# Performance work log

Hardware: AMD Instinct MI355X
Metric: run time of the kernel (lower is better)

## Reference

```python
import jax, jax.numpy as jnp
import numpy as np

N_NODES = 100000
N_EDGES = 1600000
F_IN, H1, H2, N_CLS = 512, 180, 120, 40
NEG_SLOPE = 0.01  # F.leaky_relu default


def setup_inputs() -> dict:
    key = jax.random.key(0)
    ks = jax.random.split(key, 8)
    x = jax.random.normal(ks[0], (N_NODES, F_IN), dtype=jnp.float32)
    edge_index = jax.random.randint(ks[1], (2, N_EDGES), 0, N_NODES, dtype=jnp.int64)
    W1 = jax.random.normal(ks[2], (F_IN, H1), dtype=jnp.float32) / np.sqrt(F_IN)
    b1 = jnp.zeros((H1,), dtype=jnp.float32)
    W2 = jax.random.normal(ks[3], (H1, H2), dtype=jnp.float32) / np.sqrt(H1)
    b2 = jnp.zeros((H2,), dtype=jnp.float32)
    W3 = jax.random.normal(ks[4], (H2, N_CLS), dtype=jnp.float32) / np.sqrt(H2)
    b3 = jnp.zeros((N_CLS,), dtype=jnp.float32)
    return {"x": x, "edge_index": edge_index, "W1": W1, "b1": b1,
            "W2": W2, "b2": b2, "W3": W3, "b3": b3}


def _add_self_loops(edge_index, n):
    loop = jnp.arange(n, dtype=edge_index.dtype)
    src = jnp.concatenate([edge_index[0], loop])
    dst = jnp.concatenate([edge_index[1], loop])
    return src, dst


def _gcn_conv(h, src, dst, norm, W, b, n):
    # PyG GCNConv: linear transform first, then normalized scatter-add at dst.
    h = h @ W  # [N, out]
    msg = norm[:, None] * h[src]  # gather at source, per-edge scale
    out = jax.ops.segment_sum(msg, dst, num_segments=n)  # scatter-add at dest
    return out + b


def reference(x, edge_index, W1, b1, W2, b2, W3, b3):
    n = x.shape[0]
    src, dst = _add_self_loops(edge_index, n)
    # symmetric normalization deg^-1/2 * deg^-1/2 on self-loop-augmented graph
    ones = jnp.ones(dst.shape[0], dtype=x.dtype)
    deg = jax.ops.segment_sum(ones, dst, num_segments=n)
    dinv = jnp.where(deg > 0, jax.lax.rsqrt(deg), 0.0)
    norm = dinv[src] * dinv[dst]  # [E+N]

    h = _gcn_conv(x, src, dst, norm, W1, b1, n)
    h = jnp.where(h >= 0, h, NEG_SLOPE * h)
    h = _gcn_conv(h, src, dst, norm, W2, b2, n)
    h = jnp.where(h >= 0, h, NEG_SLOPE * h)
    logits = h @ W3 + b3
    return jax.nn.log_softmax(logits, axis=1)
```

## Files before the change

kernel.cpp:

```cpp
#include <hip/hip_runtime.h>
#include <math.h>

typedef __attribute__((ext_vector_type(8))) short short8;
typedef __attribute__((ext_vector_type(4))) float f32x4;

static constexpr int F_IN = 512;
static constexpr int H1V = 180, H1P = 192;
static constexpr int H2V = 120, H2P = 128;
static constexpr int NC  = 40,  NCP = 64;

__device__ inline unsigned f2bf(float f) {
    unsigned u = __float_as_uint(f);
    return (u + 0x7fffu + ((u >> 16) & 1u)) >> 16;
}
__device__ inline unsigned cvtpk(float lo, float hi) {
    unsigned r;
    asm("v_cvt_pk_bf16_f32 %0, %1, %2" : "=v"(r) : "v"(lo), "v"(hi));
    return r;
}
#define BLO(u) __uint_as_float((u) << 16)
#define BHI(u) __uint_as_float((u) & 0xffff0000u)

__device__ inline void gload_lds16(const void* gsrc, void* ldst) {
    __builtin_amdgcn_global_load_lds(
        (const __attribute__((address_space(1))) void*)gsrc,
        (__attribute__((address_space(3))) void*)ldst, 16, 0, 0);
}

__global__ void k_detect(const int* __restrict__ ei, int* __restrict__ flag) {
    int i = blockIdx.x * 256 + threadIdx.x;
    if (ei[2 * i + 1] != 0) flag[0] = 0;
}

__global__ void k_hist(const int* __restrict__ ei, int E, const int* __restrict__ flag,
                       int* __restrict__ deg, int* __restrict__ rank) {
    int e = blockIdx.x * 256 + threadIdx.x;
    if (e >= E) return;
    int d = flag[0] ? ei[2 * E + 2 * e] : ei[E + e];
    rank[e] = atomicAdd(&deg[d], 1);
}

__global__ void k_dinv(const int* __restrict__ deg, float* __restrict__ dinv, int n) {
    int i = blockIdx.x * 256 + threadIdx.x;
    if (i < n) dinv[i] = rsqrtf((float)(deg[i] + 1));
}

__global__ void k_scan1(const int* __restrict__ deg, int* __restrict__ rp,
                        int* __restrict__ bsum, int n) {
    __shared__ int s[256];
    int t = threadIdx.x;
    int base = blockIdx.x * 1024 + t * 4;
    int v0 = (base + 0 < n) ? deg[base + 0] : 0;
    int v1 = (base + 1 < n) ? deg[base + 1] : 0;
    int v2 = (base + 2 < n) ? deg[base + 2] : 0;
    int v3 = (base + 3 < n) ? deg[base + 3] : 0;
    int sum = v0 + v1 + v2 + v3;
    s[t] = sum;
    __syncthreads();
    for (int off = 1; off < 256; off <<= 1) {
        int x = (t >= off) ? s[t - off] : 0;
        __syncthreads();
        s[t] += x;
        __syncthreads();
    }
    int run = s[t] - sum;
    if (t == 255) bsum[blockIdx.x] = s[255];
    if (base + 0 < n) rp[base + 0] = run; run += v0;
    if (base + 1 < n) rp[base + 1] = run; run += v1;
    if (base + 2 < n) rp[base + 2] = run; run += v2;
    if (base + 3 < n) rp[base + 3] = run;
}

__global__ void k_scan2(int* __restrict__ bsum, int nb) {
    __shared__ int s[128];
    int t = threadIdx.x;
    int v = (t < nb) ? bsum[t] : 0;
    s[t] = v;
    __syncthreads();
    for (int off = 1; off < 128; off <<= 1) {
        int x = (t >= off) ? s[t - off] : 0;
        __syncthreads();
        s[t] += x;
        __syncthreads();
    }
    if (t < nb) bsum[t] = s[t] - v;
}

__global__ void k_scan3(const int* __restrict__ bsum, int* __restrict__ rp,
                        int n, int E) {
    int i = blockIdx.x * 256 + threadIdx.x;
    if (i < n) {
        rp[i] = rp[i] + bsum[i >> 10];
    } else if (i == n) {
        rp[n] = E;
    }
}

__global__ __launch_bounds__(256) void k_fill(const int* __restrict__ ei, int E,
                                              const int* __restrict__ flag,
                                              const int* __restrict__ rp,
                                              const int* __restrict__ rank,
                                              int* __restrict__ csr,
                                              int bw, int chunk) {
    int bkt = blockIdx.x & 7;
    int lo = bkt * bw, hi = lo + bw;
    int ch = blockIdx.x >> 3;
    int e0 = ch * chunk;
    int e1 = min(E, e0 + chunk);
    bool i64 = flag[0] != 0;
    for (int e = e0 + (int)threadIdx.x; e < e1; e += 256) {
        int d = i64 ? ei[2 * E + 2 * e] : ei[E + e];
        if (d >= lo && d < hi) {
            int s = i64 ? ei[2 * e] : ei[e];
            csr[rp[d] + rank[e]] = s;
        }
    }
}

__global__ void k_pad(const float* __restrict__ src, float* __restrict__ dst,
                      int KS, int NS, int ND, int total) {
    int i = blockIdx.x * 256 + threadIdx.x;
    if (i >= total) return;
    int k = i / ND, nn = i % ND;
    dst[i] = (k < KS && nn < NS) ? src[k * NS + nn] : 0.0f;
}

__global__ void k_padneg(const float* __restrict__ src, float* __restrict__ dst,
                         int NS, int ND) {
    int i = threadIdx.x;
    if (i < ND) dst[i] = (i < NS) ? src[i] : -1e30f;
}

__global__ void k_prepw(const float* __restrict__ src, unsigned short* __restrict__ dst,
                        int KS, int NS, int KD, int ND) {
    int i = blockIdx.x * 256 + threadIdx.x;
    if (i >= KD * ND) return;
    int k = i / ND, c = i % ND;
    float v = (k < KS && c < NS) ? src[k * NS + c] : 0.0f;
    dst[(size_t)(k >> 3) * ND * 8 + c * 8 + (k & 7)] = (unsigned short)f2bf(v);
}

__global__ __launch_bounds__(512) void k_gemm1(const float* __restrict__ X,
                                               const short8* __restrict__ Bs,
                                               const float* __restrict__ dinv,
                                               unsigned short* __restrict__ Hout,
                                               int M) {
    __shared__ float ldsf[8192];
    char* lds = (char*)ldsf;
    int t = threadIdx.x;
    int w = t >> 6, l = t & 63;
    int lr = l & 15, kg = l >> 4;
    int wr = w >> 2, wc = w & 3;
    int row0 = blockIdx.x * 128;
    int colb = wc * 48;

    f32x4 acc[4][3];
#pragma unroll
    for (int m = 0; m < 4; ++m)
#pragma unroll
        for (int nn = 0; nn < 3; ++nn) acc[m][nn] = (f32x4){0.f, 0.f, 0.f, 0.f};

    auto stage = [&](int kb, int buf) {
#pragma unroll
        for (int j = 0; j < 2; ++j) {
            int o = j * 8192 + t * 16;
            int row = o >> 7;
            int col4 = ((o >> 4) & 7) ^ (row & 7);
            int rowg = row0 + row;
            if (rowg >= M) rowg = M - 1;
            gload_lds16(X + (size_t)rowg * F_IN + kb + col4 * 4,
                        lds + buf * 16384 + j * 8192 + w * 1024);
        }
    };

    stage(0, 0);
    __syncthreads();

    for (int ts = 0; ts < 16; ++ts) {
        int cur = ts & 1;
        if (ts < 15) stage((ts + 1) * 32, cur ^ 1);
        short8 b[3];
#pragma unroll
        for (int nn = 0; nn < 3; ++nn)
            b[nn] = Bs[(size_t)(ts * 4 + kg) * H1P + colb + nn * 16 + lr];
        short8 a[4];
#pragma unroll
        for (int m = 0; m < 4; ++m) {
            int row = wr * 64 + m * 16 + lr;
            char* base = lds + cur * 16384 + row * 128;
            float4 v0 = *(const float4*)(base + (((2 * kg + 0) ^ (row & 7)) * 16));
            float4 v1 = *(const float4*)(base + (((2 * kg + 1) ^ (row & 7)) * 16));
            union { unsigned u[4]; short8 s; } cu;
            cu.u[0] = cvtpk(v0.x, v0.y);
            cu.u[1] = cvtpk(v0.z, v0.w);
            cu.u[2] = cvtpk(v1.x, v1.y);
            cu.u[3] = cvtpk(v1.z, v1.w);
            a[m] = cu.s;
        }
#pragma unroll
        for (int m = 0; m < 4; ++m)
#pragma unroll
            for (int nn = 0; nn < 3; ++nn)
                acc[m][nn] = __builtin_amdgcn_mfma_f32_16x16x32_bf16(a[m], b[nn], acc[m][nn], 0, 0, 0);
        __syncthreads();
    }

#pragma unroll
    for (int m = 0; m < 4; ++m) {
        int r4 = row0 + wr * 64 + m * 16 + kg * 4;
#pragma unroll
        for (int j = 0; j < 4; ++j) {
            int grow = r4 + j;
            if (grow < M) {
                float dv = dinv[grow];
#pragma unroll
                for (int nn = 0; nn < 3; ++nn)
                    Hout[(size_t)grow * H1P + colb + nn * 16 + lr] =
                        (unsigned short)f2bf(acc[m][nn][j] * dv);
            }
        }
    }
}

__global__ __launch_bounds__(512) void k_gemm2(const unsigned short* __restrict__ A,
                                               const short8* __restrict__ Bs,
                                               const float* __restrict__ dinv,
                                               unsigned short* __restrict__ Hout,
                                               int M) {
    __shared__ unsigned short ldsu[16384];
    char* lds = (char*)ldsu;
    int t = threadIdx.x;
    int w = t >> 6, l = t & 63;
    int lr = l & 15, kg = l >> 4;
    int wr = w >> 2, wc = w & 3;
    int row0 = blockIdx.x * 128;
    int colb = wc * 32;

    f32x4 acc[4][2];
#pragma unroll
    for (int m = 0; m < 4; ++m)
#pragma unroll
        for (int nn = 0; nn < 2; ++nn) acc[m][nn] = (f32x4){0.f, 0.f, 0.f, 0.f};

    auto stage = [&](int kb, int buf) {
#pragma unroll
        for (int j = 0; j < 2; ++j) {
            int o = j * 8192 + t * 16;
            int row = o >> 7;
            int chunk = ((o >> 4) & 7) ^ (row & 7);
            int rowg = row0 + row;
            if (rowg >= M) rowg = M - 1;
            gload_lds16(A + (size_t)rowg * H1P + kb + chunk * 8,
                        lds + buf * 16384 + j * 8192 + w * 1024);
        }
    };

    stage(0, 0);
    __syncthreads();

    for (int ts = 0; ts < 3; ++ts) {
        int cur = ts & 1;
        if (ts < 2) stage((ts + 1) * 64, cur ^ 1);
        short8 b[2][2];
#pragma unroll
        for (int kk = 0; kk < 2; ++kk)
#pragma unroll
            for (int nn = 0; nn < 2; ++nn)
                b[kk][nn] = Bs[(size_t)(ts * 8 + kk * 4 + kg) * H2P + colb + nn * 16 + lr];
        short8 a[2][4];
#pragma unroll
        for (int kk = 0; kk < 2; ++kk)
#pragma unroll
            for (int m = 0; m < 4; ++m) {
                int row = wr * 64 + m * 16 + lr;
                a[kk][m] = *(const short8*)(lds + cur * 16384 + row * 128 +
                                            (((kk * 4 + kg) ^ (row & 7)) * 16));
            }
#pragma unroll
        for (int kk = 0; kk < 2; ++kk)
#pragma unroll
            for (int m = 0; m < 4; ++m)
#pragma unroll
                for (int nn = 0; nn < 2; ++nn)
                    acc[m][nn] = __builtin_amdgcn_mfma_f32_16x16x32_bf16(a[kk][m], b[kk][nn], acc[m][nn], 0, 0, 0);
        __syncthreads();
    }

#pragma unroll
    for (int m = 0; m < 4; ++m) {
        int r4 = row0 + wr * 64 + m * 16 + kg * 4;
#pragma unroll
        for (int j = 0; j < 4; ++j) {
            int grow = r4 + j;
            if (grow < M) {
                float dv = dinv[grow];
#pragma unroll
                for (int nn = 0; nn < 2; ++nn)
                    Hout[(size_t)grow * H2P + colb + nn * 16 + lr] =
                        (unsigned short)f2bf(acc[m][nn][j] * dv);
            }
        }
    }
}

template <int CH, int OUTBF>
__global__ __launch_bounds__(256) void k_gat(const uint2* __restrict__ H,
                                             const float* __restrict__ dinv,
                                             const int* __restrict__ rp,
                                             const int* __restrict__ csr,
                                             const float* __restrict__ bias,
                                             void* __restrict__ outv, int n) {
    int wv = threadIdx.x >> 6, l = threadIdx.x & 63;
    int i = blockIdx.x * 4 + wv;
    if (i >= n) return;
    bool act = l < CH;
    int c = act ? l : 0;
    const uint2* Hr = H + c;

    float a0, a1, a2, a3;
    {
        uint2 v = Hr[(size_t)i * CH];
        a0 = BLO(v.x); a1 = BHI(v.x); a2 = BLO(v.y); a3 = BHI(v.y);
    }
    float p0 = 0.f, p1 = 0.f, p2 = 0.f, p3 = 0.f;

    int e0 = rp[i], e1 = rp[i + 1];
    int e = e0;
    for (; e + 3 < e1; e += 4) {
        int s0 = csr[e], s1 = csr[e + 1], s2 = csr[e + 2], s3 = csr[e + 3];
        uint2 va = Hr[(size_t)s0 * CH];
        uint2 vb = Hr[(size_t)s1 * CH];
        uint2 vc = Hr[(size_t)s2 * CH];
        uint2 vd = Hr[(size_t)s3 * CH];
        a0 += BLO(va.x); a1 += BHI(va.x); a2 += BLO(va.y); a3 += BHI(va.y);
        p0 += BLO(vb.x); p1 += BHI(vb.x); p2 += BLO(vb.y); p3 += BHI(vb.y);
        a0 += BLO(vc.x); a1 += BHI(vc.x); a2 += BLO(vc.y); a3 += BHI(vc.y);
        p0 += BLO(vd.x); p1 += BHI(vd.x); p2 += BLO(vd.y); p3 += BHI(vd.y);
    }
    for (; e < e1; ++e) {
        int s0 = csr[e];
        uint2 va = Hr[(size_t)s0 * CH];
        a0 += BLO(va.x); a1 += BHI(va.x); a2 += BLO(va.y); a3 += BHI(va.y);
    }
    a0 += p0; a1 += p1; a2 += p2; a3 += p3;

    float di = dinv[i];
    float4 bb = *(const float4*)(bias + 4 * c);
    float o0 = fmaf(di, a0, bb.x);
    float o1 = fmaf(di, a1, bb.y);
    float o2 = fmaf(di, a2, bb.z);
    float o3 = fmaf(di, a3, bb.w);
    o0 = o0 >= 0.f ? o0 : 0.01f * o0;
    o1 = o1 >= 0.f ? o1 : 0.01f * o1;
    o2 = o2 >= 0.f ? o2 : 0.01f * o2;
    o3 = o3 >= 0.f ? o3 : 0.01f * o3;
    if (act) {
        if (OUTBF) {
            uint2 r;
            r.x = (f2bf(o1) << 16) | f2bf(o0);
            r.y = (f2bf(o3) << 16) | f2bf(o2);
            ((uint2*)outv)[(size_t)i * CH + c] = r;
        } else {
            ((float4*)outv)[(size_t)i * CH + c] = make_float4(o0, o1, o2, o3);
        }
    }
}

__global__ __launch_bounds__(256) void k_gat2(const uint2* __restrict__ H,
                                              const float* __restrict__ dinv,
                                              const int* __restrict__ rp,
                                              const int* __restrict__ csr,
                                              const float* __restrict__ bias,
                                              uint2* __restrict__ out, int n) {
    int wv = threadIdx.x >> 6, l = threadIdx.x & 63;
    int half = l >> 5, c = l & 31;
    int i = blockIdx.x * 8 + wv * 2 + half;
    if (i >= n) return;
    const uint2* Hr = H + c;

    float a0, a1, a2, a3;
    {
        uint2 v = Hr[(size_t)i * 32];
        a0 = BLO(v.x); a1 = BHI(v.x); a2 = BLO(v.y); a3 = BHI(v.y);
    }
    float p0 = 0.f, p1 = 0.f, p2 = 0.f, p3 = 0.f;

    int e0 = rp[i], e1 = rp[i + 1];
    int e = e0;
    for (; e + 3 < e1; e += 4) {
        int s0 = csr[e], s1 = csr[e + 1], s2 = csr[e + 2], s3 = csr[e + 3];
        uint2 va = Hr[(size_t)s0 * 32];
        uint2 vb = Hr[(size_t)s1 * 32];
        uint2 vc = Hr[(size_t)s2 * 32];
        uint2 vd = Hr[(size_t)s3 * 32];
        a0 += BLO(va.x); a1 += BHI(va.x); a2 += BLO(va.y); a3 += BHI(va.y);
        p0 += BLO(vb.x); p1 += BHI(vb.x); p2 += BLO(vb.y); p3 += BHI(vb.y);
        a0 += BLO(vc.x); a1 += BHI(vc.x); a2 += BLO(vc.y); a3 += BHI(vc.y);
        p0 += BLO(vd.x); p1 += BHI(vd.x); p2 += BLO(vd.y); p3 += BHI(vd.y);
    }
    for (; e < e1; ++e) {
        int s0 = csr[e];
        uint2 va = Hr[(size_t)s0 * 32];
        a0 += BLO(va.x); a1 += BHI(va.x); a2 += BLO(va.y); a3 += BHI(va.y);
    }
    a0 += p0; a1 += p1; a2 += p2; a3 += p3;

    float di = dinv[i];
    float4 bb = *(const float4*)(bias + 4 * c);
    float o0 = fmaf(di, a0, bb.x);
    float o1 = fmaf(di, a1, bb.y);
    float o2 = fmaf(di, a2, bb.z);
    float o3 = fmaf(di, a3, bb.w);
    o0 = o0 >= 0.f ? o0 : 0.01f * o0;
    o1 = o1 >= 0.f ? o1 : 0.01f * o1;
    o2 = o2 >= 0.f ? o2 : 0.01f * o2;
    o3 = o3 >= 0.f ? o3 : 0.01f * o3;
    uint2 r;
    r.x = (f2bf(o1) << 16) | f2bf(o0);
    r.y = (f2bf(o3) << 16) | f2bf(o2);
    out[(size_t)i * 32 + c] = r;
}

__global__ __launch_bounds__(256) void k_out(const unsigned short* __restrict__ H,
                                             const short8* __restrict__ Bs,
                                             const float* __restrict__ b3p,
                                             float* __restrict__ out, int M) {
    int t = threadIdx.x;
    int w = t >> 6, l = t & 63;
    int lr = l & 15, kg = l >> 4;
    int row0 = blockIdx.x * 64 + w * 16;

    f32x4 acc[4];
#pragma unroll
    for (int f = 0; f < 4; ++f) acc[f] = (f32x4){0.f, 0.f, 0.f, 0.f};

    int rowa = row0 + lr;
    if (rowa >= M) rowa = M - 1;
    const unsigned short* arow = H + (size_t)rowa * H2P;

#pragma unroll
    for (int ks = 0; ks < 4; ++ks) {
        short8 a = *(const short8*)(arow + ks * 32 + kg * 8);
#pragma unroll
        for (int f = 0; f < 4; ++f) {
            short8 b = Bs[(size_t)(ks * 4 + kg) * NCP + f * 16 + lr];
            acc[f] = __builtin_amdgcn_mfma_f32_16x16x32_bf16(a, b, acc[f], 0, 0, 0);
        }
    }

    float bl[4];
#pragma unroll
    for (int f = 0; f < 4; ++f) bl[f] = b3p[f * 16 + lr];

#pragma unroll
    for (int j = 0; j < 4; ++j) {
        int grow = row0 + kg * 4 + j;
        float lg[4];
#pragma unroll
        for (int f = 0; f < 4; ++f) lg[f] = acc[f][j] + bl[f];
        float m = fmaxf(fmaxf(lg[0], lg[1]), fmaxf(lg[2], lg[3]));
#pragma unroll
        for (int d = 1; d < 16; d <<= 1) m = fmaxf(m, __shfl_xor(m, d));
        float s = expf(lg[0] - m) + expf(lg[1] - m) + expf(lg[2] - m) + expf(lg[3] - m);
#pragma unroll
        for (int d = 1; d < 16; d <<= 1) s += __shfl_xor(s, d);
        float lse = m + logf(s);
        if (grow < M) {
#pragma unroll
            for (int f = 0; f < 4; ++f) {
                int c = f * 16 + lr;
                if (c < NC) out[(size_t)grow * NC + c] = lg[f] - lse;
            }
        }
    }
}

extern "C" void kernel_launch(void* const* d_in, const int* in_sizes, int n_in,
                              void* d_out, int out_size, void* d_ws, size_t ws_size,
                              hipStream_t stream) {
    const float* x  = (const float*)d_in[0];
    const int*   ei = (const int*)d_in[1];
    const float* W1 = (const float*)d_in[2];
    const float* b1 = (const float*)d_in[3];
    const float* W2 = (const float*)d_in[4];
    const float* b2 = (const float*)d_in[5];
    const float* W3 = (const float*)d_in[6];
    const float* b3 = (const float*)d_in[7];
    float* outp = (float*)d_out;

    int n = in_sizes[0] / F_IN;
    int E = in_sizes[1] / 2;

    char* p = (char*)d_ws;
    auto alloc = [&](size_t bytes) -> char* {
        char* r = p;
        p += (bytes + 511) & ~(size_t)511;
        return r;
    };
    int*            flag   = (int*)alloc(4);
    int*            deg    = (int*)alloc((size_t)n * 4);
    float*          dinv   = (float*)alloc((size_t)n * 4);
    int*            rp     = (int*)alloc((size_t)(n + 1) * 4);
    int*            bsum   = (int*)alloc(4096);
    int*            rank   = (int*)alloc((size_t)E * 4);
    int*            csr    = (int*)alloc((size_t)E * 4);
    unsigned short* W1s    = (unsigned short*)alloc((size_t)F_IN * H1P * 2);
    unsigned short* W2s    = (unsigned short*)alloc((size_t)H1P * H2P * 2);
    unsigned short* W3s    = (unsigned short*)alloc((size_t)H2P * NCP * 2);
    float*          b1p    = (float*)alloc(H1P * 4);
    float*          b2p    = (float*)alloc(H2P * 4);
    float*          b3p    = (float*)alloc(NCP * 4);
    unsigned short* h1     = (unsigned short*)alloc((size_t)n * H1P * 2);
    unsigned short* h1agg  = (unsigned short*)alloc((size_t)n * H1P * 2);
    unsigned short* h2     = (unsigned short*)alloc((size_t)n * H2P * 2);
    unsigned short* h2agg  = (unsigned short*)alloc((size_t)n * H2P * 2);

    hipMemsetAsync(flag, 1, 4, stream);
    hipMemsetAsync(deg, 0, (size_t)n * 4, stream);

    k_detect<<<16, 256, 0, stream>>>(ei, flag);

    int eb = (E + 255) / 256;
    k_hist<<<eb, 256, 0, stream>>>(ei, E, flag, deg, rank);
    k_dinv<<<(n + 255) / 256, 256, 0, stream>>>(deg, dinv, n);

    int nb = (n + 1023) / 1024;
    k_scan1<<<nb, 256, 0, stream>>>(deg, rp, bsum, n);
    k_scan2<<<1, 128, 0, stream>>>(bsum, nb);
    k_scan3<<<(n + 1 + 255) / 256, 256, 0, stream>>>(bsum, rp, n, E);

    int bw = (n + 7) / 8;
    int nch = 256;
    int chunk = (E + nch - 1) / nch;
    k_fill<<<nch * 8, 256, 0, stream>>>(ei, E, flag, rp, rank, csr, bw, chunk);

    k_prepw<<<(F_IN * H1P + 255) / 256, 256, 0, stream>>>(W1, W1s, F_IN, H1V, F_IN, H1P);
    k_prepw<<<(H1P * H2P + 255) / 256, 256, 0, stream>>>(W2, W2s, H1V, H2V, H1P, H2P);
    k_prepw<<<(H2P * NCP + 255) / 256, 256, 0, stream>>>(W3, W3s, H2V, NC, H2P, NCP);
    k_pad<<<1, 256, 0, stream>>>(b1, b1p, 1, H1V, H1P, H1P);
    k_pad<<<1, 256, 0, stream>>>(b2, b2p, 1, H2V, H2P, H2P);
    k_padneg<<<1, 64, 0, stream>>>(b3, b3p, NC, NCP);

    int gb = (n + 127) / 128;
    k_gemm1<<<gb, 512, 0, stream>>>(x, (const short8*)W1s, dinv, h1, n);
    k_gat<H1P / 4, 1><<<(n + 3) / 4, 256, 0, stream>>>((const uint2*)h1, dinv, rp, csr, b1p, h1agg, n);
    k_gemm2<<<gb, 512, 0, stream>>>(h1agg, (const short8*)W2s, dinv, h2, n);
    k_gat2<<<(n + 7) / 8, 256, 0, stream>>>((const uint2*)h2, dinv, rp, csr, b2p, (uint2*)h2agg, n);
    k_out<<<(n + 63) / 64, 256, 0, stream>>>(h2agg, (const short8*)W3s, b3p, outp, n);
}
```

Baseline: 395.2 us.

## Fuse neighbor aggregation with following GEMM via LDS staging

```diff
diff --git a/kernel.cpp b/kernel.cpp
--- a/kernel.cpp
+++ b/kernel.cpp
@@ -222,225 +222,169 @@
     }
 }
 
-__global__ __launch_bounds__(512) void k_gemm2(const unsigned short* __restrict__ A,
+__global__ __launch_bounds__(256) void k_fuse2(const uint2* __restrict__ H,
+                                               const float* __restrict__ dinv,
+                                               const int* __restrict__ rp,
+                                               const int* __restrict__ csr,
+                                               const float* __restrict__ bias,
                                                const short8* __restrict__ Bs,
-                                               const float* __restrict__ dinv,
                                                unsigned short* __restrict__ Hout,
-                                               int M) {
-    __shared__ unsigned short ldsu[16384];
-    char* lds = (char*)ldsu;
+                                               int n) {
+    __shared__ float ldsf[6400];
+    char* lds = (char*)ldsf;
     int t = threadIdx.x;
     int w = t >> 6, l = t & 63;
-    int lr = l & 15, kg = l >> 4;
-    int wr = w >> 2, wc = w & 3;
-    int row0 = blockIdx.x * 128;
-    int colb = wc * 32;
-
-    f32x4 acc[4][2];
-#pragma unroll
-    for (int m = 0; m < 4; ++m)
-#pragma unroll
-        for (int nn = 0; nn < 2; ++nn) acc[m][nn] = (f32x4){0.f, 0.f, 0.f, 0.f};
-
-    auto stage = [&](int kb, int buf) {
-#pragma unroll
-        for (int j = 0; j < 2; ++j) {
-            int o = j * 8192 + t * 16;
-            int row = o >> 7;
-            int chunk = ((o >> 4) & 7) ^ (row & 7);
-            int rowg = row0 + row;
-            if (rowg >= M) rowg = M - 1;
-            gload_lds16(A + (size_t)rowg * H1P + kb + chunk * 8,
-                        lds + buf * 16384 + j * 8192 + w * 1024);
-        }
-    };
-
-    stage(0, 0);
-    __syncthreads();
-
-    for (int ts = 0; ts < 3; ++ts) {
-        int cur = ts & 1;
-        if (ts < 2) stage((ts + 1) * 64, cur ^ 1);
-        short8 b[2][2];
-#pragma unroll
-        for (int kk = 0; kk < 2; ++kk)
-#pragma unroll
-            for (int nn = 0; nn < 2; ++nn)
-                b[kk][nn] = Bs[(size_t)(ts * 8 + kk * 4 + kg) * H2P + colb + nn * 16 + lr];
-        short8 a[2][4];
-#pragma unroll
-        for (int kk = 0; kk < 2; ++kk)
-#pragma unroll
-            for (int m = 0; m < 4; ++m) {
-                int row = wr * 64 + m * 16 + lr;
-                a[kk][m] = *(const short8*)(lds + cur * 16384 + row * 128 +
-                                            (((kk * 4 + kg) ^ (row & 7)) * 16));
-            }
-#pragma unroll
-        for (int kk = 0; kk < 2; ++kk)
-#pragma unroll
-            for (int m = 0; m < 4; ++m)
-#pragma unroll
-                for (int nn = 0; nn < 2; ++nn)
-                    acc[m][nn] = __builtin_amdgcn_mfma_f32_16x16x32_bf16(a[kk][m], b[kk][nn], acc[m][nn], 0, 0, 0);
-        __syncthreads();
-    }
-
-#pragma unroll
-    for (int m = 0; m < 4; ++m) {
-        int r4 = row0 + wr * 64 + m * 16 + kg * 4;
-#pragma unroll
-        for (int j = 0; j < 4; ++j) {
-            int grow = r4 + j;
-            if (grow < M) {
-                float dv = dinv[grow];
-#pragma unroll
-                for (int nn = 0; nn < 2; ++nn)
-                    Hout[(size_t)grow * H2P + colb + nn * 16 + lr] =
-                        (unsigned short)f2bf(acc[m][nn][j] * dv);
-            }
-        }
-    }
-}
-
-template <int CH, int OUTBF>
-__global__ __launch_bounds__(256) void k_gat(const uint2* __restrict__ H,
-                                             const float* __restrict__ dinv,
-                                             const int* __restrict__ rp,
-                                             const int* __restrict__ csr,
-                                             const float* __restrict__ bias,
-                                             void* __restrict__ outv, int n) {
-    int wv = threadIdx.x >> 6, l = threadIdx.x & 63;
-    int i = blockIdx.x * 4 + wv;
-    if (i >= n) return;
-    bool act = l < CH;
+    int row0 = blockIdx.x * 64;
+
+    bool act = l < 48;
     int c = act ? l : 0;
     const uint2* Hr = H + c;
-
-    float a0, a1, a2, a3;
-    {
-        uint2 v = Hr[(size_t)i * CH];
-        a0 = BLO(v.x); a1 = BHI(v.x); a2 = BLO(v.y); a3 = BHI(v.y);
-    }
-    float p0 = 0.f, p1 = 0.f, p2 = 0.f, p3 = 0.f;
-
-    int e0 = rp[i], e1 = rp[i + 1];
-    int e = e0;
-    for (; e + 3 < e1; e += 4) {
-        int s0 = csr[e], s1 = csr[e + 1], s2 = csr[e + 2], s3 = csr[e + 3];
-        uint2 va = Hr[(size_t)s0 * CH];
-        uint2 vb = Hr[(size_t)s1 * CH];
-        uint2 vc = Hr[(size_t)s2 * CH];
-        uint2 vd = Hr[(size_t)s3 * CH];
-        a0 += BLO(va.x); a1 += BHI(va.x); a2 += BLO(va.y); a3 += BHI(va.y);
-        p0 += BLO(vb.x); p1 += BHI(vb.x); p2 += BLO(vb.y); p3 += BHI(vb.y);
-        a0 += BLO(vc.x); a1 += BHI(vc.x); a2 += BLO(vc.y); a3 += BHI(vc.y);
-        p0 += BLO(vd.x); p1 += BHI(vd.x); p2 += BLO(vd.y); p3 += BHI(vd.y);
-    }
-    for (; e < e1; ++e) {
-        int s0 = csr[e];
-        uint2 va = Hr[(size_t)s0 * CH];
-        a0 += BLO(va.x); a1 += BHI(va.x); a2 += BLO(va.y); a3 += BHI(va.y);
-    }
-    a0 += p0; a1 += p1; a2 += p2; a3 += p3;
-
-    float di = dinv[i];
     float4 bb = *(const float4*)(bias + 4 * c);
-    float o0 = fmaf(di, a0, bb.x);
-    float o1 = fmaf(di, a1, bb.y);
-    float o2 = fmaf(di, a2, bb.z);
-    float o3 = fmaf(di, a3, bb.w);
-    o0 = o0 >= 0.f ? o0 : 0.01f * o0;
-    o1 = o1 >= 0.f ? o1 : 0.01f * o1;
-    o2 = o2 >= 0.f ? o2 : 0.01f * o2;
-    o3 = o3 >= 0.f ? o3 : 0.01f * o3;
-    if (act) {
-        if (OUTBF) {
+
+    for (int j = 0; j < 16; ++j) {
+        int i = row0 + w * 16 + j;
+        if (i >= n) break;
+        float a0, a1, a2, a3;
+        {
+            uint2 v = Hr[(size_t)i * 48];
+            a0 = BLO(v.x); a1 = BHI(v.x); a2 = BLO(v.y); a3 = BHI(v.y);
+        }
+        float p0 = 0.f, p1 = 0.f, p2 = 0.f, p3 = 0.f;
+        int e0 = rp[i], e1 = rp[i + 1];
+        int e = e0;
+        for (; e + 3 < e1; e += 4) {
+            int s0 = csr[e], s1 = csr[e + 1], s2 = csr[e + 2], s3 = csr[e + 3];
+            uint2 va = Hr[(size_t)s0 * 48];
+            uint2 vb = Hr[(size_t)s1 * 48];
+            uint2 vc = Hr[(size_t)s2 * 48];
+            uint2 vd = Hr[(size_t)s3 * 48];
+            a0 += BLO(va.x); a1 += BHI(va.x); a2 += BLO(va.y); a3 += BHI(va.y);
+            p0 += BLO(vb.x); p1 += BHI(vb.x); p2 += BLO(vb.y); p3 += BHI(vb.y);
+            a0 += BLO(vc.x); a1 += BHI(vc.x); a2 += BLO(vc.y); a3 += BHI(vc.y);
+            p0 += BLO(vd.x); p1 += BHI(vd.x); p2 += BLO(vd.y); p3 += BHI(vd.y);
+        }
+        for (; e < e1; ++e) {
+            int s0 = csr[e];
+            uint2 va = Hr[(size_t)s0 * 48];
+            a0 += BLO(va.x); a1 += BHI(va.x); a2 += BLO(va.y); a3 += BHI(va.y);
+        }
+        a0 += p0; a1 += p1; a2 += p2; a3 += p3;
+        float di = dinv[i];
+        float o0 = fmaf(di, a0, bb.x);
+        float o1 = fmaf(di, a1, bb.y);
+        float o2 = fmaf(di, a2, bb.z);
+        float o3 = fmaf(di, a3, bb.w);
+        o0 = o0 >= 0.f ? o0 : 0.01f * o0;
+        o1 = o1 >= 0.f ? o1 : 0.01f * o1;
+        o2 = o2 >= 0.f ? o2 : 0.01f * o2;
+        o3 = o3 >= 0.f ? o3 : 0.01f * o3;
+        if (act) {
             uint2 r;
             r.x = (f2bf(o1) << 16) | f2bf(o0);
             r.y = (f2bf(o3) << 16) | f2bf(o2);
-            ((uint2*)outv)[(size_t)i * CH + c] = r;
-        } else {
-            ((float4*)outv)[(size_t)i * CH + c] = make_float4(o0, o1, o2, o3);
-        }
-    }
-}
-
-__global__ __launch_bounds__(256) void k_gat2(const uint2* __restrict__ H,
-                                              const float* __restrict__ dinv,
-                                              const int* __restrict__ rp,
-                                              const int* __restrict__ csr,
-                                              const float* __restrict__ bias,
-                                              uint2* __restrict__ out, int n) {
-    int wv = threadIdx.x >> 6, l = threadIdx.x & 63;
-    int half = l >> 5, c = l & 31;
-    int i = blockIdx.x * 8 + wv * 2 + half;
-    if (i >= n) return;
-    const uint2* Hr = H + c;
-
-    float a0, a1, a2, a3;
-    {
-        uint2 v = Hr[(size_t)i * 32];
-        a0 = BLO(v.x); a1 = BHI(v.x); a2 = BLO(v.y); a3 = BHI(v.y);
-    }
-    float p0 = 0.f, p1 = 0.f, p2 = 0.f, p3 = 0.f;
-
-    int e0 = rp[i], e1 = rp[i + 1];
-    int e = e0;
-    for (; e + 3 < e1; e += 4) {
-        int s0 = csr[e], s1 = csr[e + 1], s2 = csr[e + 2], s3 = csr[e + 3];
-        uint2 va = Hr[(size_t)s0 * 32];
-        uint2 vb = Hr[(size_t)s1 * 32];
-        uint2 vc = Hr[(size_t)s2 * 32];
-        uint2 vd = Hr[(size_t)s3 * 32];
-        a0 += BLO(va.x); a1 += BHI(va.x); a2 += BLO(va.y); a3 += BHI(va.y);
-        p0 += BLO(vb.x); p1 += BHI(vb.x); p2 += BLO(vb.y); p3 += BHI(vb.y);
-        a0 += BLO(vc.x); a1 += BHI(vc.x); a2 += BLO(vc.y); a3 += BHI(vc.y);
-        p0 += BLO(vd.x); p1 += BHI(vd.x); p2 += BLO(vd.y); p3 += BHI(vd.y);
-    }
-    for (; e < e1; ++e) {
-        int s0 = csr[e];
-        uint2 va = Hr[(size_t)s0 * 32];
-        a0 += BLO(va.x); a1 += BHI(va.x); a2 += BLO(va.y); a3 += BHI(va.y);
-    }
-    a0 += p0; a1 += p1; a2 += p2; a3 += p3;
-
-    float di = dinv[i];
-    float4 bb = *(const float4*)(bias + 4 * c);
-    float o0 = fmaf(di, a0, bb.x);
-    float o1 = fmaf(di, a1, bb.y);
-    float o2 = fmaf(di, a2, bb.z);
-    float o3 = fmaf(di, a3, bb.w);
-    o0 = o0 >= 0.f ? o0 : 0.01f * o0;
-    o1 = o1 >= 0.f ? o1 : 0.01f * o1;
-    o2 = o2 >= 0.f ? o2 : 0.01f * o2;
-    o3 = o3 >= 0.f ? o3 : 0.01f * o3;
-    uint2 r;
-    r.x = (f2bf(o1) << 16) | f2bf(o0);
-    r.y = (f2bf(o3) << 16) | f2bf(o2);
-    out[(size_t)i * 32 + c] = r;
-}
-
-__global__ __launch_bounds__(256) void k_out(const unsigned short* __restrict__ H,
-                                             const short8* __restrict__ Bs,
-                                             const float* __restrict__ b3p,
-                                             float* __restrict__ out, int M) {
+            *(uint2*)(lds + (w * 16 + j) * 400 + c * 8) = r;
+        }
+    }
+    __syncthreads();
+
+    int lr = l & 15, kg = l >> 4;
+    f32x4 acc[8];
+#pragma unroll
+    for (int f = 0; f < 8; ++f) acc[f] = (f32x4){0.f, 0.f, 0.f, 0.f};
+
+#pragma unroll
+    for (int ks = 0; ks < 6; ++ks) {
+        short8 a = *(const short8*)(lds + (w * 16 + lr) * 400 + ks * 64 + kg * 16);
+#pragma unroll
+        for (int f = 0; f < 8; ++f) {
+            short8 b = Bs[(size_t)(ks * 4 + kg) * H2P + f * 16 + lr];
+            acc[f] = __builtin_amdgcn_mfma_f32_16x16x32_bf16(a, b, acc[f], 0, 0, 0);
+        }
+    }
+
+#pragma unroll
+    for (int j = 0; j < 4; ++j) {
+        int grow = row0 + w * 16 + kg * 4 + j;
+        if (grow < n) {
+            float dv = dinv[grow];
+#pragma unroll
+            for (int f = 0; f < 8; ++f)
+                Hout[(size_t)grow * H2P + f * 16 + lr] =
+                    (unsigned short)f2bf(acc[f][j] * dv);
+        }
+    }
+}
+
+__global__ __launch_bounds__(256) void k_fuse3(const uint2* __restrict__ H,
+                                               const float* __restrict__ dinv,
+                                               const int* __restrict__ rp,
+                                               const int* __restrict__ csr,
+                                               const float* __restrict__ bias,
+                                               const short8* __restrict__ Bs,
+                                               const float* __restrict__ b3p,
+                                               float* __restrict__ out, int n) {
+    __shared__ float ldsf[4352];
+    char* lds = (char*)ldsf;
     int t = threadIdx.x;
     int w = t >> 6, l = t & 63;
+    int row0 = blockIdx.x * 64;
+
+    int half = l >> 5, cc = l & 31;
+    const uint2* Hr = H + cc;
+    float4 bb = *(const float4*)(bias + 4 * cc);
+
+    for (int jj = 0; jj < 8; ++jj) {
+        int i = row0 + w * 16 + jj * 2 + half;
+        if (i >= n) continue;
+        float a0, a1, a2, a3;
+        {
+            uint2 v = Hr[(size_t)i * 32];
+            a0 = BLO(v.x); a1 = BHI(v.x); a2 = BLO(v.y); a3 = BHI(v.y);
+        }
+        float p0 = 0.f, p1 = 0.f, p2 = 0.f, p3 = 0.f;
+        int e0 = rp[i], e1 = rp[i + 1];
+        int e = e0;
+        for (; e + 3 < e1; e += 4) {
+            int s0 = csr[e], s1 = csr[e + 1], s2 = csr[e + 2], s3 = csr[e + 3];
+            uint2 va = Hr[(size_t)s0 * 32];
+            uint2 vb = Hr[(size_t)s1 * 32];
+            uint2 vc = Hr[(size_t)s2 * 32];
+            uint2 vd = Hr[(size_t)s3 * 32];
+            a0 += BLO(va.x); a1 += BHI(va.x); a2 += BLO(va.y); a3 += BHI(va.y);
+            p0 += BLO(vb.x); p1 += BHI(vb.x); p2 += BLO(vb.y); p3 += BHI(vb.y);
+            a0 += BLO(vc.x); a1 += BHI(vc.x); a2 += BLO(vc.y); a3 += BHI(vc.y);
+            p0 += BLO(vd.x); p1 += BHI(vd.x); p2 += BLO(vd.y); p3 += BHI(vd.y);
+        }
+        for (; e < e1; ++e) {
+            int s0 = csr[e];
+            uint2 va = Hr[(size_t)s0 * 32];
+            a0 += BLO(va.x); a1 += BHI(va.x); a2 += BLO(va.y); a3 += BHI(va.y);
+        }
+        a0 += p0; a1 += p1; a2 += p2; a3 += p3;
+        float di = dinv[i];
+        float o0 = fmaf(di, a0, bb.x);
+        float o1 = fmaf(di, a1, bb.y);
+        float o2 = fmaf(di, a2, bb.z);
+        float o3 = fmaf(di, a3, bb.w);
+        o0 = o0 >= 0.f ? o0 : 0.01f * o0;
+        o1 = o1 >= 0.f ? o1 : 0.01f * o1;
+        o2 = o2 >= 0.f ? o2 : 0.01f * o2;
+        o3 = o3 >= 0.f ? o3 : 0.01f * o3;
+        uint2 r;
+        r.x = (f2bf(o1) << 16) | f2bf(o0);
+        r.y = (f2bf(o3) << 16) | f2bf(o2);
+        *(uint2*)(lds + (w * 16 + jj * 2 + half) * 272 + cc * 8) = r;
+    }
+    __syncthreads();
+
     int lr = l & 15, kg = l >> 4;
-    int row0 = blockIdx.x * 64 + w * 16;
-
     f32x4 acc[4];
 #pragma unroll
     for (int f = 0; f < 4; ++f) acc[f] = (f32x4){0.f, 0.f, 0.f, 0.f};
 
-    int rowa = row0 + lr;
-    if (rowa >= M) rowa = M - 1;
-    const unsigned short* arow = H + (size_t)rowa * H2P;
-
 #pragma unroll
     for (int ks = 0; ks < 4; ++ks) {
-        short8 a = *(const short8*)(arow + ks * 32 + kg * 8);
+        short8 a = *(const short8*)(lds + (w * 16 + lr) * 272 + ks * 64 + kg * 16);
 #pragma unroll
         for (int f = 0; f < 4; ++f) {
             short8 b = Bs[(size_t)(ks * 4 + kg) * NCP + f * 16 + lr];
@@ -454,7 +398,7 @@
 
 #pragma unroll
     for (int j = 0; j < 4; ++j) {
-        int grow = row0 + kg * 4 + j;
+        int grow = row0 + w * 16 + kg * 4 + j;
         float lg[4];
 #pragma unroll
         for (int f = 0; f < 4; ++f) lg[f] = acc[f][j] + bl[f];
@@ -465,7 +409,7 @@
 #pragma unroll
         for (int d = 1; d < 16; d <<= 1) s += __shfl_xor(s, d);
         float lse = m + logf(s);
-        if (grow < M) {
+        if (grow < n) {
 #pragma unroll
             for (int f = 0; f < 4; ++f) {
                 int c = f * 16 + lr;
@@ -511,9 +455,7 @@
     float*          b2p    = (float*)alloc(H2P * 4);
     float*          b3p    = (float*)alloc(NCP * 4);
     unsigned short* h1     = (unsigned short*)alloc((size_t)n * H1P * 2);
-    unsigned short* h1agg  = (unsigned short*)alloc((size_t)n * H1P * 2);
     unsigned short* h2     = (unsigned short*)alloc((size_t)n * H2P * 2);
-    unsigned short* h2agg  = (unsigned short*)alloc((size_t)n * H2P * 2);
 
     hipMemsetAsync(flag, 1, 4, stream);
     hipMemsetAsync(deg, 0, (size_t)n * 4, stream);
@@ -543,8 +485,8 @@
 
     int gb = (n + 127) / 128;
     k_gemm1<<<gb, 512, 0, stream>>>(x, (const short8*)W1s, dinv, h1, n);
-    k_gat<H1P / 4, 1><<<(n + 3) / 4, 256, 0, stream>>>((const uint2*)h1, dinv, rp, csr, b1p, h1agg, n);
-    k_gemm2<<<gb, 512, 0, stream>>>(h1agg, (const short8*)W2s, dinv, h2, n);
-    k_gat2<<<(n + 7) / 8, 256, 0, stream>>>((const uint2*)h2, dinv, rp, csr, b2p, (uint2*)h2agg, n);
-    k_out<<<(n + 63) / 64, 256, 0, stream>>>(h2agg, (const short8*)W3s, b3p, outp, n);
-}
+    k_fuse2<<<(n + 63) / 64, 256, 0, stream>>>((const uint2*)h1, dinv, rp, csr, b1p,
+                                               (const short8*)W2s, h2, n);
+    k_fuse3<<<(n + 63) / 64, 256, 0, stream>>>((const uint2*)h2, dinv, rp, csr, b2p,
+                                               (const short8*)W3s, b3p, outp, n);
+}
```

New measurement: 430.0 us. +8.8%, slower.
